# Kernel optimization log

Measured on AMD Instinct MI355X. Metric: run time of the kernel, lower is better.

## Reference

```python
import jax, jax.numpy as jnp
import numpy as np

N, H2, T = 64, 1024, 512  # num steps/documents, 2*hidden_dim, tokens per step
EPS = 1e-12  # torch F.normalize eps


def setup_inputs() -> dict:
    key = jax.random.key(0)
    k1, k2, k3, k4 = jax.random.split(key, 4)
    return {
        "hidden_states": jax.random.normal(k1, (N, H2, T), dtype=jnp.float32),
        "W_attention": jax.random.normal(k2, (H2, H2), dtype=jnp.float32),
        "bias_attention": jax.random.normal(k3, (H2,), dtype=jnp.float32),
        "u_w0": jax.random.normal(k4, (H2,), dtype=jnp.float32),
    }


def reference(hidden_states, W_attention, bias_attention, u_w0):
    n = hidden_states.shape[0]

    # Sequential recurrence on u_w: u_w <- normalize(u_w @ W^T + b), updated
    # BEFORE being used at each step i. Collect the post-update value per step.
    def step(u, _):
        u_new = u @ W_attention.T + bias_attention
        u_new = u_new / jnp.maximum(jnp.linalg.norm(u_new), EPS)
        return u_new, u_new

    _, u_ws = jax.lax.scan(step, u_w0, None, length=n)  # (N, 2H)

    # u_it = tanh(h_i^T W^T + b) for all steps, batched: (N, T, 2H)
    u_it = jnp.tanh(jnp.einsum('ndt,ed->nte', hidden_states, W_attention)
                    + bias_attention)

    # attention scores per step, softmax over the T axis (torch Softmax(dim=0)
    # on a (T,1) column)
    scores = jnp.einsum('nte,ne->nt', u_it, u_ws)  # (N, T)
    a = jax.nn.softmax(scores, axis=1)

    # weighted sum s_i = h_i @ a_i -> stacked as rows: (N, 2H)
    s = jnp.einsum('ndt,nt->nd', hidden_states, a)
    return s
```

## Files before the change

### kernel.cpp

```cpp
#include <hip/hip_runtime.h>
#include <cstdint>
#include <cstddef>

#define H2 1024
#define TT 512
#define NSTEPS 64
#define RBLK 32
#define RTHR 512

using floatx4 = __attribute__((__ext_vector_type__(4))) float;
using half8   = __attribute__((__ext_vector_type__(8))) _Float16;
using half4   = __attribute__((__ext_vector_type__(4))) _Float16;
typedef unsigned long long u64;

__device__ __forceinline__ float tanh_fast(float x) {
  return 1.0f - 2.0f / (__expf(2.0f * x) + 1.0f);
}

#define GLDS16(gp, lp)                                                         \
  __builtin_amdgcn_global_load_lds(                                            \
      (const __attribute__((address_space(1))) void*)(gp),                     \
      (__attribute__((address_space(3))) void*)(lp), 16, 0, 0)

__global__ __launch_bounds__(RTHR, 1) void recur_kernel(
    const float* __restrict__ W, const float* __restrict__ bias,
    const float* __restrict__ u0, float* __restrict__ vbuf,
    float* __restrict__ norm2) {
  __shared__ __align__(16) float ub[2][H2 + 64];
  __shared__ float bredn[2];
  int tid = threadIdx.x;
  int row = tid >> 4, g = tid & 15;
  int r = blockIdx.x * RBLK + row;
  int w = tid >> 6, l = tid & 63;

  floatx4 wreg[16];
  {
    const floatx4* wr = (const floatx4*)(W + ((size_t)r << 10) + (g << 6));
#pragma unroll
    for (int j = 0; j < 16; ++j) wreg[j] = wr[j];
  }
#pragma unroll
  for (int j = 0; j < 16; ++j) asm volatile("" : "+v"(wreg[j]));
  float bl = bias[r];

  for (int i = 0; i < NSTEPS; ++i) {
    float* cb = ub[i & 1];
    float rs;
    if (i == 0) {
      int f = 2 * tid;
      int addr = f + 4 * (f >> 6);
      float2 v2 = *(const float2*)(u0 + f);
      *(float2*)(cb + addr) = v2;
      __syncthreads();
      rs = 1.0f;
    } else {
      if (w == 0) {
        const u64* src = (const u64*)(vbuf + ((size_t)(i - 1) << 10)) + l;
        u64 v[8];
        for (;;) {
          bool ok = true;
#pragma unroll
          for (int j = 0; j < 8; ++j) {
            v[j] = __hip_atomic_load(src + 64 * j, __ATOMIC_RELAXED,
                                     __HIP_MEMORY_SCOPE_AGENT);
            ok &= ((unsigned)(v[j] & 0xFFFFFFFFu) != 0xFFFFFFFFu) &
                  ((unsigned)(v[j] >> 32) != 0xFFFFFFFFu);
          }
          if (__all(ok)) break;
          __builtin_amdgcn_s_sleep(1);
        }
        float sq = 0.f;
#pragma unroll
        for (int j = 0; j < 8; ++j) {
          int F0 = 2 * l + 128 * j;
          int addr = F0 + 4 * (F0 >> 6);
          *(u64*)(cb + addr) = v[j];
          float f0 = __builtin_bit_cast(float, (unsigned)(v[j] & 0xFFFFFFFFu));
          float f1 = __builtin_bit_cast(float, (unsigned)(v[j] >> 32));
          sq += f0 * f0 + f1 * f1;
        }
#pragma unroll
        for (int off = 1; off <= 32; off <<= 1) sq += __shfl_xor(sq, off, 64);
        if (l == 0) bredn[i & 1] = sq;
      }
      __syncthreads();
      float nrm = bredn[i & 1];
      rs = 1.0f / fmaxf(sqrtf(nrm), 1e-12f);
      if (blockIdx.x == 0 && tid == 64) norm2[i - 1] = nrm;
    }

    const floatx4* ug = (const floatx4*)(cb + 68 * g);
    float acc = 0.f;
#pragma unroll
    for (int j = 0; j < 16; ++j) {
      floatx4 a = wreg[j], c = ug[j];
      acc += a.x * c.x + a.y * c.y + a.z * c.z + a.w * c.w;
    }
#pragma unroll
    for (int off = 1; off <= 8; off <<= 1) acc += __shfl_xor(acc, off, 64);

    if (g == 0) {
      float yv = acc * rs + bl;
      __hip_atomic_store(vbuf + ((size_t)i << 10) + r, yv, __ATOMIC_RELAXED,
                         __HIP_MEMORY_SCOPE_AGENT);
    }
  }

  if (blockIdx.x == 0 && w == 0) {
    const u64* src = (const u64*)(vbuf + ((size_t)(NSTEPS - 1) << 10)) + l;
    u64 v[8];
    for (;;) {
      bool ok = true;
#pragma unroll
      for (int j = 0; j < 8; ++j) {
        v[j] = __hip_atomic_load(src + 64 * j, __ATOMIC_RELAXED,
                                 __HIP_MEMORY_SCOPE_AGENT);
        ok &= ((unsigned)(v[j] & 0xFFFFFFFFu) != 0xFFFFFFFFu) &
              ((unsigned)(v[j] >> 32) != 0xFFFFFFFFu);
      }
      if (__all(ok)) break;
      __builtin_amdgcn_s_sleep(1);
    }
    float sq = 0.f;
#pragma unroll
    for (int j = 0; j < 8; ++j) {
      float f0 = __builtin_bit_cast(float, (unsigned)(v[j] & 0xFFFFFFFFu));
      float f1 = __builtin_bit_cast(float, (unsigned)(v[j] >> 32));
      sq += f0 * f0 + f1 * f1;
    }
#pragma unroll
    for (int off = 1; off <= 32; off <<= 1) sq += __shfl_xor(sq, off, 64);
    if (l == 0) norm2[NSTEPS - 1] = sq;
  }
}

__global__ __launch_bounds__(256) void wconv_kernel(const float* __restrict__ W,
                                                    _Float16* __restrict__ Wh) {
  int i = blockIdx.x * 256 + threadIdx.x;
  float4 v = ((const float4*)W)[i];
  half4 o = {(_Float16)v.x, (_Float16)v.y, (_Float16)v.z, (_Float16)v.w};
  ((half4*)Wh)[i] = o;
}

__global__ __launch_bounds__(256) void transpose_h(const float* __restrict__ h,
                                                   _Float16* __restrict__ hhT) {
  int n = blockIdx.z, d0 = blockIdx.x * 64, t0 = blockIdx.y * 64;
  __shared__ float tile[64][65];
  const float* hb = h + ((size_t)n * H2 + d0) * TT + t0;
  int dr = threadIdx.x >> 4, tc = (threadIdx.x & 15) << 2;
#pragma unroll
  for (int p = 0; p < 4; ++p) {
    float4 v = *(const float4*)(hb + (size_t)(dr + p * 16) * TT + tc);
    tile[dr + p * 16][tc] = v.x;
    tile[dr + p * 16][tc + 1] = v.y;
    tile[dr + p * 16][tc + 2] = v.z;
    tile[dr + p * 16][tc + 3] = v.w;
  }
  __syncthreads();
  _Float16* ob = hhT + ((size_t)n * TT + t0) * H2 + d0;
  int tr = threadIdx.x >> 3, seg = threadIdx.x & 7;
#pragma unroll
  for (int p = 0; p < 2; ++p) {
    int t = tr + p * 32;
    half8 hv;
#pragma unroll
    for (int u = 0; u < 8; ++u) hv[u] = (_Float16)tile[seg * 8 + u][t];
    *(half8*)(ob + (size_t)t * H2 + seg * 8) = hv;
  }
}

__global__ __launch_bounds__(256) void gemm2(
    const _Float16* __restrict__ Wh, const _Float16* __restrict__ hhT,
    const float* __restrict__ bias, const float* __restrict__ vbuf,
    const float* __restrict__ norm2, float* __restrict__ scores) {
  int x = blockIdx.x;
  int xcd = x & 7, slot = x >> 3;
  int e_t = slot & 7;
  int tn = xcd * 32 + (slot >> 3);
  int t_t = tn & 3, n = tn >> 2;
  int e_base = e_t * 128, t_base = t_t * 128;

  int tid = threadIdx.x, lane = tid & 63, w = tid >> 6;
  int q = lane >> 4, m = lane & 15;
  int eoff = (w & 1) * 64, toff = (w >> 1) * 64;

  __shared__ __align__(16) _Float16 Ash[128 * 32];
  __shared__ __align__(16) _Float16 Bsh[128 * 32];

  floatx4 zero = {0.f, 0.f, 0.f, 0.f};
  floatx4 acc[4][4];
#pragma unroll
  for (int i = 0; i < 4; ++i)
#pragma unroll
    for (int j = 0; j < 4; ++j) acc[i][j] = zero;

  int rl = lane >> 2, kseg = lane & 3;
  const _Float16* gA0 =
      Wh + (((size_t)(e_base + w * 32 + rl)) << 10) + kseg * 8;
  const _Float16* gA1 = gA0 + ((size_t)16 << 10);
  const _Float16* gB0 = hhT + ((size_t)n << 19) +
                        (((size_t)(t_base + w * 32 + rl)) << 10) + kseg * 8;
  const _Float16* gB1 = gB0 + ((size_t)16 << 10);
  _Float16* lA0 = Ash + (w * 32) * 32;
  _Float16* lA1 = lA0 + 16 * 32;
  _Float16* lB0 = Bsh + (w * 32) * 32;
  _Float16* lB1 = lB0 + 16 * 32;

  for (int k0 = 0; k0 < H2; k0 += 32) {
    GLDS16(gA0 + k0, lA0);
    GLDS16(gA1 + k0, lA1);
    GLDS16(gB0 + k0, lB0);
    GLDS16(gB1 + k0, lB1);
    __syncthreads();

    half8 af[4], bf[4];
#pragma unroll
    for (int i = 0; i < 4; ++i)
      af[i] = *(const half8*)&Ash[(eoff + i * 16 + m) * 32 + q * 8];
#pragma unroll
    for (int j = 0; j < 4; ++j)
      bf[j] = *(const half8*)&Bsh[(toff + j * 16 + m) * 32 + q * 8];
#pragma unroll
    for (int i = 0; i < 4; ++i)
#pragma unroll
      for (int j = 0; j < 4; ++j)
        acc[i][j] =
            __builtin_amdgcn_mfma_f32_16x16x32_f16(af[i], bf[j], acc[i][j], 0, 0, 0);
    __syncthreads();
  }

  float* uloc = (float*)Ash;
  float* bloc = uloc + 128;
  if (tid < 128) {
    float rsn = 1.0f / fmaxf(sqrtf(norm2[n]), 1e-12f);
    uloc[tid] = vbuf[((size_t)n << 10) + e_base + tid] * rsn;
    bloc[tid] = bias[e_base + tid];
  }
  __syncthreads();

  float part[4] = {0.f, 0.f, 0.f, 0.f};
#pragma unroll
  for (int i = 0; i < 4; ++i) {
#pragma unroll
    for (int reg = 0; reg < 4; ++reg) {
      int el = eoff + i * 16 + q * 4 + reg;
      float ubv = uloc[el];
      float bbv = bloc[el];
#pragma unroll
      for (int j = 0; j < 4; ++j) {
        float y = acc[i][j][reg] + bbv;
        part[j] += tanh_fast(y) * ubv;
      }
    }
  }
#pragma unroll
  for (int j = 0; j < 4; ++j) {
    part[j] += __shfl_xor(part[j], 16, 64);
    part[j] += __shfl_xor(part[j], 32, 64);
    if (lane < 16) {
      int t = t_base + toff + j * 16 + lane;
      atomicAdd(&scores[(size_t)n * TT + t], part[j]);
    }
  }
}

__global__ __launch_bounds__(256) void out_kernel(
    const float* __restrict__ h, const float* __restrict__ scores,
    float* __restrict__ out) {
  int n = blockIdx.y;
  int ds = blockIdx.x;
  int tid = threadIdx.x;
  int w = tid >> 6, lane = tid & 63;

  __shared__ float sa[TT];
  __shared__ float wred[8];

  float s0 = scores[(size_t)n * TT + tid];
  float s1 = scores[(size_t)n * TT + 256 + tid];

  float mx = fmaxf(s0, s1);
#pragma unroll
  for (int off = 32; off >= 1; off >>= 1) mx = fmaxf(mx, __shfl_xor(mx, off, 64));
  if (lane == 0) wred[w] = mx;
  __syncthreads();
  mx = fmaxf(fmaxf(wred[0], wred[1]), fmaxf(wred[2], wred[3]));

  float e0 = __expf(s0 - mx);
  float e1 = __expf(s1 - mx);
  float ssum = e0 + e1;
#pragma unroll
  for (int off = 32; off >= 1; off >>= 1) ssum += __shfl_xor(ssum, off, 64);
  if (lane == 0) wred[4 + w] = ssum;
  __syncthreads();
  ssum = wred[4] + wred[5] + wred[6] + wred[7];
  float inv = 1.0f / ssum;
  sa[tid] = e0 * inv;
  sa[tid + 256] = e1 * inv;
  __syncthreads();

  int d0 = ds * 64 + w * 16;
  const float4* hb = reinterpret_cast<const float4*>(h + (size_t)n * H2 * TT);
#pragma unroll 1
  for (int rr = 0; rr < 16; ++rr) {
    int d = d0 + rr;
    const float4* hr = hb + (size_t)d * (TT / 4);
    float4 a4 = hr[lane];
    float4 b4 = hr[64 + lane];
    int t0 = 4 * lane;
    float acc = a4.x * sa[t0] + a4.y * sa[t0 + 1] + a4.z * sa[t0 + 2] +
                a4.w * sa[t0 + 3] + b4.x * sa[256 + t0] +
                b4.y * sa[256 + t0 + 1] + b4.z * sa[256 + t0 + 2] +
                b4.w * sa[256 + t0 + 3];
#pragma unroll
    for (int off = 1; off <= 32; off <<= 1) acc += __shfl_xor(acc, off, 64);
    if (lane == 0) out[(size_t)n * H2 + d] = acc;
  }
}

extern "C" void kernel_launch(void* const* d_in, const int* in_sizes, int n_in,
                              void* d_out, int out_size, void* d_ws, size_t ws_size,
                              hipStream_t stream) {
  const float* h    = (const float*)d_in[0];
  const float* W    = (const float*)d_in[1];
  const float* bias = (const float*)d_in[2];
  const float* u0   = (const float*)d_in[3];
  float* out = (float*)d_out;

  float* wsf    = (float*)d_ws;
  float* norm2  = wsf;
  float* scores = wsf + 64;
  float* vbuf   = wsf + 64 + NSTEPS * TT;
  unsigned* ctr = (unsigned*)(vbuf + (size_t)NSTEPS * H2);
  float* after_ctr = (float*)(ctr + 16);
  size_t fixed_floats = (size_t)(after_ctr - wsf);
  _Float16* Wh  = (_Float16*)after_ctr;
  _Float16* hhT = Wh + (size_t)H2 * H2;
  size_t need = fixed_floats * 4 + (size_t)H2 * H2 * 2 +
                (size_t)NSTEPS * TT * H2 * 2;
  bool big = ws_size >= need;

  hipMemsetAsync(d_ws, 0, (size_t)(64 + NSTEPS * TT) * sizeof(float), stream);
  hipMemsetAsync(vbuf, 0xFF, (size_t)NSTEPS * H2 * sizeof(float), stream);

  {
    const float* Wp = W; const float* bp = bias; const float* up = u0;
    float* vp = vbuf; float* np = norm2;
    void* kargs[] = {&Wp, &bp, &up, &vp, &np};
    hipLaunchCooperativeKernel((void*)recur_kernel, dim3(RBLK), dim3(RTHR),
                               kargs, 0, stream);
  }

  if (big) {
    wconv_kernel<<<dim3(H2 * H2 / 1024), dim3(256), 0, stream>>>(W, Wh);
    transpose_h<<<dim3(16, 8, 64), dim3(256), 0, stream>>>(h, hhT);
    gemm2<<<dim3(2048), dim3(256), 0, stream>>>(Wh, hhT, bias, vbuf, norm2,
                                                scores);
  } else {
    gemm2<<<dim3(2048), dim3(256), 0, stream>>>(Wh, hhT, bias, vbuf, norm2,
                                                scores);
  }

  out_kernel<<<dim3(16, 64), dim3(256), 0, stream>>>(h, scores, out);

  (void)in_sizes; (void)n_in; (void)out_size; (void)ws_size;
}
```

Before: 507.6 us.

## Fuse W/h fp16 preprocessing into the cooperative recurrence kernel to overlap

Merges the W fp32-to-fp16 conversion and the h transpose/convert into the cooperative recurrence launch as 224 extra blocks. These blocks run concurrently with the 32 serial recurrence blocks, hiding the latency-bound recurrence behind the bandwidth-bound preprocessing and removing two launches. The recurrence is also remapped so each wavefront owns 4 rows with a full-wave shuffle reduction and packed 64-bit stores, and the s_sleep in the polling loops is dropped. Risks: the preprocessing traffic may contend with the latency-sensitive recurrence polling, and the workspace-size fallback path is removed.

```diff
diff --git a/kernel.cpp b/kernel.cpp
--- a/kernel.cpp
+++ b/kernel.cpp
@@ -7,6 +7,8 @@
 #define NSTEPS 64
 #define RBLK 32
 #define RTHR 512
+#define PREBLK 224
+#define TOTBLK (RBLK + PREBLK)
 
 using floatx4 = __attribute__((__ext_vector_type__(4))) float;
 using half8   = __attribute__((__ext_vector_type__(8))) _Float16;
@@ -22,150 +24,183 @@
       (const __attribute__((address_space(1))) void*)(gp),                     \
       (__attribute__((address_space(3))) void*)(lp), 16, 0, 0)
 
-__global__ __launch_bounds__(RTHR, 1) void recur_kernel(
+__global__ __launch_bounds__(RTHR, 1) void recur_pre_kernel(
     const float* __restrict__ W, const float* __restrict__ bias,
     const float* __restrict__ u0, float* __restrict__ vbuf,
-    float* __restrict__ norm2) {
-  __shared__ __align__(16) float ub[2][H2 + 64];
-  __shared__ float bredn[2];
+    float* __restrict__ norm2, _Float16* __restrict__ Wh,
+    const float* __restrict__ h, _Float16* __restrict__ hhT) {
+  __shared__ __align__(16) char smem[2 * 16640];
   int tid = threadIdx.x;
-  int row = tid >> 4, g = tid & 15;
-  int r = blockIdx.x * RBLK + row;
-  int w = tid >> 6, l = tid & 63;
-
-  floatx4 wreg[16];
-  {
-    const floatx4* wr = (const floatx4*)(W + ((size_t)r << 10) + (g << 6));
-#pragma unroll
-    for (int j = 0; j < 16; ++j) wreg[j] = wr[j];
-  }
-#pragma unroll
-  for (int j = 0; j < 16; ++j) asm volatile("" : "+v"(wreg[j]));
-  float bl = bias[r];
-
-  for (int i = 0; i < NSTEPS; ++i) {
-    float* cb = ub[i & 1];
-    float rs;
-    if (i == 0) {
-      int f = 2 * tid;
-      int addr = f + 4 * (f >> 6);
-      float2 v2 = *(const float2*)(u0 + f);
-      *(float2*)(cb + addr) = v2;
+
+  if (blockIdx.x < RBLK) {
+    float* ub = (float*)smem;
+    float* bredn = (float*)(smem + 8192);
+    int w = tid >> 6, l = tid & 63;
+    int r0 = blockIdx.x * RBLK + w * 4;
+
+    floatx4 wreg[16];
+    float blv[4];
+#pragma unroll
+    for (int p = 0; p < 4; ++p) {
+      const float* wr = W + ((size_t)(r0 + p) << 10) + 4 * l;
+#pragma unroll
+      for (int j = 0; j < 4; ++j)
+        wreg[p * 4 + j] = *(const floatx4*)(wr + 256 * j);
+      blv[p] = bias[r0 + p];
+    }
+#pragma unroll
+    for (int j = 0; j < 16; ++j) asm volatile("" : "+v"(wreg[j]));
+
+    for (int i = 0; i < NSTEPS; ++i) {
+      float* cb = ub + (i & 1) * 1024;
+      float rs;
+      if (i == 0) {
+        if (w == 0) {
+#pragma unroll
+          for (int j = 0; j < 4; ++j) {
+            floatx4 v = *((const floatx4*)u0 + l + 64 * j);
+            *(floatx4*)(cb + 4 * l + 256 * j) = v;
+          }
+        }
+        __syncthreads();
+        rs = 1.0f;
+      } else {
+        if (w == 0) {
+          const u64* src = (const u64*)(vbuf + ((size_t)(i - 1) << 10)) + l;
+          u64 v[8];
+          for (;;) {
+            bool ok = true;
+#pragma unroll
+            for (int j = 0; j < 8; ++j) {
+              v[j] = __hip_atomic_load(src + 64 * j, __ATOMIC_RELAXED,
+                                       __HIP_MEMORY_SCOPE_AGENT);
+              ok &= ((unsigned)(v[j] & 0xFFFFFFFFu) != 0xFFFFFFFFu) &
+                    ((unsigned)(v[j] >> 32) != 0xFFFFFFFFu);
+            }
+            if (__all(ok)) break;
+          }
+          float sq = 0.f;
+#pragma unroll
+          for (int j = 0; j < 8; ++j) {
+            *(u64*)(cb + 2 * l + 128 * j) = v[j];
+            float f0 =
+                __builtin_bit_cast(float, (unsigned)(v[j] & 0xFFFFFFFFu));
+            float f1 = __builtin_bit_cast(float, (unsigned)(v[j] >> 32));
+            sq += f0 * f0 + f1 * f1;
+          }
+#pragma unroll
+          for (int off = 1; off <= 32; off <<= 1)
+            sq += __shfl_xor(sq, off, 64);
+          if (l == 0) bredn[i & 1] = sq;
+        }
+        __syncthreads();
+        float nrm = bredn[i & 1];
+        rs = 1.0f / fmaxf(sqrtf(nrm), 1e-12f);
+        if (blockIdx.x == 0 && tid == 64) norm2[i - 1] = nrm;
+      }
+
+      float acc0 = 0.f, acc1 = 0.f, acc2 = 0.f, acc3 = 0.f;
+#pragma unroll
+      for (int j = 0; j < 4; ++j) {
+        floatx4 zv = *(const floatx4*)(cb + 256 * j + 4 * l);
+        floatx4 w0 = wreg[0 * 4 + j], w1 = wreg[1 * 4 + j];
+        floatx4 w2 = wreg[2 * 4 + j], w3 = wreg[3 * 4 + j];
+        acc0 += w0.x * zv.x + w0.y * zv.y + w0.z * zv.z + w0.w * zv.w;
+        acc1 += w1.x * zv.x + w1.y * zv.y + w1.z * zv.z + w1.w * zv.w;
+        acc2 += w2.x * zv.x + w2.y * zv.y + w2.z * zv.z + w2.w * zv.w;
+        acc3 += w3.x * zv.x + w3.y * zv.y + w3.z * zv.z + w3.w * zv.w;
+      }
+#pragma unroll
+      for (int off = 1; off <= 32; off <<= 1) {
+        acc0 += __shfl_xor(acc0, off, 64);
+        acc1 += __shfl_xor(acc1, off, 64);
+        acc2 += __shfl_xor(acc2, off, 64);
+        acc3 += __shfl_xor(acc3, off, 64);
+      }
+      if (l == 0) {
+        float y0 = acc0 * rs + blv[0], y1 = acc1 * rs + blv[1];
+        float y2 = acc2 * rs + blv[2], y3 = acc3 * rs + blv[3];
+        u64 a01 = ((u64)__builtin_bit_cast(unsigned, y1) << 32) |
+                  (u64)__builtin_bit_cast(unsigned, y0);
+        u64 a23 = ((u64)__builtin_bit_cast(unsigned, y3) << 32) |
+                  (u64)__builtin_bit_cast(unsigned, y2);
+        u64* dst = (u64*)(vbuf + ((size_t)i << 10) + r0);
+        __hip_atomic_store(dst, a01, __ATOMIC_RELAXED,
+                           __HIP_MEMORY_SCOPE_AGENT);
+        __hip_atomic_store(dst + 1, a23, __ATOMIC_RELAXED,
+                           __HIP_MEMORY_SCOPE_AGENT);
+      }
+    }
+
+    if (blockIdx.x == 0 && w == 0) {
+      const u64* src = (const u64*)(vbuf + ((size_t)(NSTEPS - 1) << 10)) + l;
+      u64 v[8];
+      for (;;) {
+        bool ok = true;
+#pragma unroll
+        for (int j = 0; j < 8; ++j) {
+          v[j] = __hip_atomic_load(src + 64 * j, __ATOMIC_RELAXED,
+                                   __HIP_MEMORY_SCOPE_AGENT);
+          ok &= ((unsigned)(v[j] & 0xFFFFFFFFu) != 0xFFFFFFFFu) &
+                ((unsigned)(v[j] >> 32) != 0xFFFFFFFFu);
+        }
+        if (__all(ok)) break;
+      }
+      float sq = 0.f;
+#pragma unroll
+      for (int j = 0; j < 8; ++j) {
+        float f0 = __builtin_bit_cast(float, (unsigned)(v[j] & 0xFFFFFFFFu));
+        float f1 = __builtin_bit_cast(float, (unsigned)(v[j] >> 32));
+        sq += f0 * f0 + f1 * f1;
+      }
+#pragma unroll
+      for (int off = 1; off <= 32; off <<= 1) sq += __shfl_xor(sq, off, 64);
+      if (l == 0) norm2[NSTEPS - 1] = sq;
+    }
+  } else {
+    int pb = blockIdx.x - RBLK;
+
+    const floatx4* Wv = (const floatx4*)W;
+    for (int idx = pb * RTHR + tid; idx < H2 * H2 / 4; idx += PREBLK * RTHR) {
+      floatx4 v = Wv[idx];
+      half4 o = {(_Float16)v.x, (_Float16)v.y, (_Float16)v.z, (_Float16)v.w};
+      ((half4*)Wh)[idx] = o;
+    }
+
+    int sub = tid >> 8, ltid = tid & 255;
+    float(*tile)[65] = (float(*)[65])(smem + sub * 16640);
+    int dr = ltid >> 4, tc = (ltid & 15) << 2;
+    int tr = ltid >> 3, seg = ltid & 7;
+    for (int base = pb * 2; base < 8192; base += PREBLK * 2) {
+      int tidx = base + sub;
+      bool act = tidx < 8192;
+      int n = tidx >> 7, rem = tidx & 127;
+      int d0 = (rem & 15) << 6, t0 = ((rem >> 4) & 7) << 6;
+      if (act) {
+        const float* hb = h + ((size_t)n * H2 + d0) * TT + t0;
+#pragma unroll
+        for (int p = 0; p < 4; ++p) {
+          floatx4 v = *(const floatx4*)(hb + (size_t)(dr + p * 16) * TT + tc);
+          tile[dr + p * 16][tc] = v.x;
+          tile[dr + p * 16][tc + 1] = v.y;
+          tile[dr + p * 16][tc + 2] = v.z;
+          tile[dr + p * 16][tc + 3] = v.w;
+        }
+      }
       __syncthreads();
-      rs = 1.0f;
-    } else {
-      if (w == 0) {
-        const u64* src = (const u64*)(vbuf + ((size_t)(i - 1) << 10)) + l;
-        u64 v[8];
-        for (;;) {
-          bool ok = true;
-#pragma unroll
-          for (int j = 0; j < 8; ++j) {
-            v[j] = __hip_atomic_load(src + 64 * j, __ATOMIC_RELAXED,
-                                     __HIP_MEMORY_SCOPE_AGENT);
-            ok &= ((unsigned)(v[j] & 0xFFFFFFFFu) != 0xFFFFFFFFu) &
-                  ((unsigned)(v[j] >> 32) != 0xFFFFFFFFu);
-          }
-          if (__all(ok)) break;
-          __builtin_amdgcn_s_sleep(1);
-        }
-        float sq = 0.f;
-#pragma unroll
-        for (int j = 0; j < 8; ++j) {
-          int F0 = 2 * l + 128 * j;
-          int addr = F0 + 4 * (F0 >> 6);
-          *(u64*)(cb + addr) = v[j];
-          float f0 = __builtin_bit_cast(float, (unsigned)(v[j] & 0xFFFFFFFFu));
-          float f1 = __builtin_bit_cast(float, (unsigned)(v[j] >> 32));
-          sq += f0 * f0 + f1 * f1;
-        }
-#pragma unroll
-        for (int off = 1; off <= 32; off <<= 1) sq += __shfl_xor(sq, off, 64);
-        if (l == 0) bredn[i & 1] = sq;
+      if (act) {
+        _Float16* ob = hhT + ((size_t)n * TT + t0) * H2 + d0;
+#pragma unroll
+        for (int p = 0; p < 2; ++p) {
+          int t = tr + p * 32;
+          half8 hv;
+#pragma unroll
+          for (int u = 0; u < 8; ++u) hv[u] = (_Float16)tile[seg * 8 + u][t];
+          *(half8*)(ob + (size_t)t * H2 + seg * 8) = hv;
+        }
       }
       __syncthreads();
-      float nrm = bredn[i & 1];
-      rs = 1.0f / fmaxf(sqrtf(nrm), 1e-12f);
-      if (blockIdx.x == 0 && tid == 64) norm2[i - 1] = nrm;
-    }
-
-    const floatx4* ug = (const floatx4*)(cb + 68 * g);
-    float acc = 0.f;
-#pragma unroll
-    for (int j = 0; j < 16; ++j) {
-      floatx4 a = wreg[j], c = ug[j];
-      acc += a.x * c.x + a.y * c.y + a.z * c.z + a.w * c.w;
-    }
-#pragma unroll
-    for (int off = 1; off <= 8; off <<= 1) acc += __shfl_xor(acc, off, 64);
-
-    if (g == 0) {
-      float yv = acc * rs + bl;
-      __hip_atomic_store(vbuf + ((size_t)i << 10) + r, yv, __ATOMIC_RELAXED,
-                         __HIP_MEMORY_SCOPE_AGENT);
-    }
-  }
-
-  if (blockIdx.x == 0 && w == 0) {
-    const u64* src = (const u64*)(vbuf + ((size_t)(NSTEPS - 1) << 10)) + l;
-    u64 v[8];
-    for (;;) {
-      bool ok = true;
-#pragma unroll
-      for (int j = 0; j < 8; ++j) {
-        v[j] = __hip_atomic_load(src + 64 * j, __ATOMIC_RELAXED,
-                                 __HIP_MEMORY_SCOPE_AGENT);
-        ok &= ((unsigned)(v[j] & 0xFFFFFFFFu) != 0xFFFFFFFFu) &
-              ((unsigned)(v[j] >> 32) != 0xFFFFFFFFu);
-      }
-      if (__all(ok)) break;
-      __builtin_amdgcn_s_sleep(1);
-    }
-    float sq = 0.f;
-#pragma unroll
-    for (int j = 0; j < 8; ++j) {
-      float f0 = __builtin_bit_cast(float, (unsigned)(v[j] & 0xFFFFFFFFu));
-      float f1 = __builtin_bit_cast(float, (unsigned)(v[j] >> 32));
-      sq += f0 * f0 + f1 * f1;
-    }
-#pragma unroll
-    for (int off = 1; off <= 32; off <<= 1) sq += __shfl_xor(sq, off, 64);
-    if (l == 0) norm2[NSTEPS - 1] = sq;
-  }
-}
-
-__global__ __launch_bounds__(256) void wconv_kernel(const float* __restrict__ W,
-                                                    _Float16* __restrict__ Wh) {
-  int i = blockIdx.x * 256 + threadIdx.x;
-  float4 v = ((const float4*)W)[i];
-  half4 o = {(_Float16)v.x, (_Float16)v.y, (_Float16)v.z, (_Float16)v.w};
-  ((half4*)Wh)[i] = o;
-}
-
-__global__ __launch_bounds__(256) void transpose_h(const float* __restrict__ h,
-                                                   _Float16* __restrict__ hhT) {
-  int n = blockIdx.z, d0 = blockIdx.x * 64, t0 = blockIdx.y * 64;
-  __shared__ float tile[64][65];
-  const float* hb = h + ((size_t)n * H2 + d0) * TT + t0;
-  int dr = threadIdx.x >> 4, tc = (threadIdx.x & 15) << 2;
-#pragma unroll
-  for (int p = 0; p < 4; ++p) {
-    float4 v = *(const float4*)(hb + (size_t)(dr + p * 16) * TT + tc);
-    tile[dr + p * 16][tc] = v.x;
-    tile[dr + p * 16][tc + 1] = v.y;
-    tile[dr + p * 16][tc + 2] = v.z;
-    tile[dr + p * 16][tc + 3] = v.w;
-  }
-  __syncthreads();
-  _Float16* ob = hhT + ((size_t)n * TT + t0) * H2 + d0;
-  int tr = threadIdx.x >> 3, seg = threadIdx.x & 7;
-#pragma unroll
-  for (int p = 0; p < 2; ++p) {
-    int t = tr + p * 32;
-    half8 hv;
-#pragma unroll
-    for (int u = 0; u < 8; ++u) hv[u] = (_Float16)tile[seg * 8 + u][t];
-    *(half8*)(ob + (size_t)t * H2 + seg * 8) = hv;
+    }
   }
 }
 
@@ -332,12 +367,8 @@
   float* vbuf   = wsf + 64 + NSTEPS * TT;
   unsigned* ctr = (unsigned*)(vbuf + (size_t)NSTEPS * H2);
   float* after_ctr = (float*)(ctr + 16);
-  size_t fixed_floats = (size_t)(after_ctr - wsf);
   _Float16* Wh  = (_Float16*)after_ctr;
   _Float16* hhT = Wh + (size_t)H2 * H2;
-  size_t need = fixed_floats * 4 + (size_t)H2 * H2 * 2 +
-                (size_t)NSTEPS * TT * H2 * 2;
-  bool big = ws_size >= need;
 
   hipMemsetAsync(d_ws, 0, (size_t)(64 + NSTEPS * TT) * sizeof(float), stream);
   hipMemsetAsync(vbuf, 0xFF, (size_t)NSTEPS * H2 * sizeof(float), stream);
@@ -345,21 +376,14 @@
   {
     const float* Wp = W; const float* bp = bias; const float* up = u0;
     float* vp = vbuf; float* np = norm2;
-    void* kargs[] = {&Wp, &bp, &up, &vp, &np};
-    hipLaunchCooperativeKernel((void*)recur_kernel, dim3(RBLK), dim3(RTHR),
-                               kargs, 0, stream);
-  }
-
-  if (big) {
-    wconv_kernel<<<dim3(H2 * H2 / 1024), dim3(256), 0, stream>>>(W, Wh);
-    transpose_h<<<dim3(16, 8, 64), dim3(256), 0, stream>>>(h, hhT);
-    gemm2<<<dim3(2048), dim3(256), 0, stream>>>(Wh, hhT, bias, vbuf, norm2,
-                                                scores);
-  } else {
-    gemm2<<<dim3(2048), dim3(256), 0, stream>>>(Wh, hhT, bias, vbuf, norm2,
-                                                scores);
-  }
-
+    _Float16* whp = Wh; const float* hp = h; _Float16* htp = hhT;
+    void* kargs[] = {&Wp, &bp, &up, &vp, &np, &whp, &hp, &htp};
+    hipLaunchCooperativeKernel((void*)recur_pre_kernel, dim3(TOTBLK),
+                               dim3(RTHR), kargs, 0, stream);
+  }
+
+  gemm2<<<dim3(2048), dim3(256), 0, stream>>>(Wh, hhT, bias, vbuf, norm2,
+                                              scores);
   out_kernel<<<dim3(16, 64), dim3(256), 0, stream>>>(h, scores, out);
 
   (void)in_sizes; (void)n_in; (void)out_size; (void)ws_size;
```

Measured after the change: 520.7 us. +2.6%, slower.
